# Kernel tuning notes

Hardware: AMD Instinct MI355X
Metric: run time of the kernel (lower is better)

The kernel has to match this reference:

```python
import jax, jax.numpy as jnp
import numpy as np

BS, C_IN, C_OUT, K, STYLE_DIM, BANK = 8, 64, 64, 3, 512, 4
D = H = W = 32
EPS = 1e-8
STRIDE = 1
PAD = 1


def setup_inputs() -> dict:
    key = jax.random.key(0)
    ks = jax.random.split(key, 7)
    lim_f = 1.0 / np.sqrt(STYLE_DIM)
    return {
        "x": jax.random.normal(ks[0], (BS, C_IN, D, H, W), dtype=jnp.float32),
        "w": jax.random.normal(ks[1], (BS, STYLE_DIM), dtype=jnp.float32),
        "filter_w": jax.random.uniform(ks[2], (BANK, STYLE_DIM), jnp.float32, -lim_f, lim_f),
        "filter_b": jax.random.uniform(ks[3], (BANK,), jnp.float32, -lim_f, lim_f),
        "mod_w": jax.random.uniform(ks[4], (C_IN, STYLE_DIM), jnp.float32, -lim_f, lim_f),
        "mod_b": jax.random.uniform(ks[5], (C_IN,), jnp.float32, -lim_f, lim_f),
        "bank": jax.random.normal(ks[6], (BANK, C_OUT, C_IN, K, K, K), dtype=jnp.float32),
    }


def reference(x, w, filter_w, filter_b, mod_w, mod_b, bank):
    bs, c_in, d, h, ww = x.shape
    # bank selection weights: softmax over bank axis
    fwt = jax.nn.softmax(w @ filter_w.T + filter_b, axis=-1)          # [bs, bank]
    # per-sample weights from bank (bank layout: n, out, in, k, k, k)
    weighted = jnp.einsum('bn,noijkl->boijkl', fwt, bank)             # [bs, out, in, k, k, k]
    # style modulation over input channels
    mod = (w @ mod_w.T + mod_b).reshape(bs, 1, c_in, 1, 1, 1)
    mw = weighted * mod
    # demodulation: normalize each (sample, out-channel) filter
    demod = jax.lax.rsqrt(jnp.sum(mw * mw, axis=(2, 3, 4, 5), keepdims=True) + EPS)
    mw = mw * demod
    # grouped conv with groups = bs
    mw = mw.reshape(bs * C_OUT, c_in, K, K, K)
    xr = x.reshape(1, bs * c_in, d, h, ww)
    out = jax.lax.conv_general_dilated(
        xr, mw,
        window_strides=(STRIDE,) * 3,
        padding=[(PAD, PAD)] * 3,
        dimension_numbers=('NCDHW', 'OIDHW', 'NCDHW'),
        feature_group_count=bs,
    )
    return out.reshape(bs, C_OUT, out.shape[-3], out.shape[-2], out.shape[-1])
```

## Files before the change

kernel.cpp:

```cpp
#include <hip/hip_runtime.h>
#include <math.h>

#define BS 8
#define CIN 64
#define COUT 64
#define SDIM 512
#define NBANK 4
#define DSZ 32
#define SPATIAL (DSZ*DSZ*DSZ)
#define NTAP 27
#define CH 8
#define NCH 8
#define KPAD 232
#define NKS 7
constexpr float EPS = 1e-8f;

typedef short bf16x8 __attribute__((ext_vector_type(8)));
typedef float f32x4 __attribute__((ext_vector_type(4)));

#define WA_ELEMS (BS*NCH*COUT*KPAD)

__device__ inline unsigned short bf16r(float f) {
    unsigned u = __float_as_uint(f);
    u = (u + 0x7fffu + ((u >> 16) & 1u)) >> 16;
    return (unsigned short)u;
}
__device__ inline unsigned pack2(float a, float b) {
    unsigned ua = __float_as_uint(a);
    unsigned ub = __float_as_uint(b);
    ua = (ua + 0x7fffu + ((ua >> 16) & 1u)) >> 16;
    ub = (ub + 0x7fffu + ((ub >> 16) & 1u)) & 0xffff0000u;
    return ua | ub;
}

__global__ void prep_style(const float* __restrict__ w,
                           const float* __restrict__ filter_w,
                           const float* __restrict__ filter_b,
                           const float* __restrict__ mod_w,
                           const float* __restrict__ mod_b,
                           float* __restrict__ fwt,
                           float* __restrict__ mod) {
    const int b = blockIdx.x;
    const int t = threadIdx.x;
    const float* wb = w + b * SDIM;
    __shared__ float lg[NBANK];

    if (t < NBANK) {
        float s = filter_b[t];
        const float* fr = filter_w + t * SDIM;
        for (int j = 0; j < SDIM; ++j) s += wb[j] * fr[j];
        lg[t] = s;
    }
    __syncthreads();
    if (t == 0) {
        float m = lg[0];
        for (int n = 1; n < NBANK; ++n) m = fmaxf(m, lg[n]);
        float e[NBANK];
        float s = 0.0f;
        for (int n = 0; n < NBANK; ++n) { e[n] = expf(lg[n] - m); s += e[n]; }
        for (int n = 0; n < NBANK; ++n) fwt[b * NBANK + n] = e[n] / s;
    }
    {
        float s = mod_b[t];
        const float* mr = mod_w + t * SDIM;
        for (int j = 0; j < SDIM; ++j) s += wb[j] * mr[j];
        mod[b * CIN + t] = s;
    }
}

__global__ void prep_weights(const float* __restrict__ bank,
                             const float* __restrict__ fwt,
                             const float* __restrict__ mod,
                             unsigned short* __restrict__ wA) {
    const int oc = blockIdx.x;
    const int b  = blockIdx.y;
    const int ic = threadIdx.x;

    const float f0 = fwt[b * NBANK + 0];
    const float f1 = fwt[b * NBANK + 1];
    const float f2 = fwt[b * NBANK + 2];
    const float f3 = fwt[b * NBANK + 3];
    const float m  = mod[b * CIN + ic];

    const float* b0 = bank + (size_t)((0 * COUT + oc) * CIN + ic) * NTAP;
    const float* b1 = bank + (size_t)((1 * COUT + oc) * CIN + ic) * NTAP;
    const float* b2 = bank + (size_t)((2 * COUT + oc) * CIN + ic) * NTAP;
    const float* b3 = bank + (size_t)((3 * COUT + oc) * CIN + ic) * NTAP;

    float v[NTAP];
    float ss = 0.0f;
#pragma unroll
    for (int k = 0; k < NTAP; ++k) {
        float t = f0 * b0[k] + f1 * b1[k] + f2 * b2[k] + f3 * b3[k];
        t *= m;
        v[k] = t;
        ss += t * t;
    }
#pragma unroll
    for (int off = 32; off >= 1; off >>= 1) ss += __shfl_xor(ss, off, 64);
    const float d = rsqrtf(ss + EPS);

    const int chunk = ic >> 3, icl = ic & 7;
    unsigned short* row = wA + (size_t)(((b * NCH + chunk) * COUT) + oc) * KPAD;
#pragma unroll
    for (int k = 0; k < NTAP; ++k) row[k * CH + icl] = bf16r(v[k] * d);

    unsigned short* rz = wA + (size_t)(((b * NCH + chunk) * COUT) + oc) * KPAD;
    rz[216 + icl * 2]     = 0;
    rz[216 + icl * 2 + 1] = 0;
}

__global__ __launch_bounds__(512, 2) void conv3d_mfma(
        const float* __restrict__ x,
        const unsigned short* __restrict__ wA,
        float* __restrict__ out) {
    const int bid = blockIdx.x;
    const int b = bid & 7, z = bid >> 3;
    const int t  = threadIdx.x;
    const int ln = t & 15;
    const int hi = (t >> 4) & 3;
    const int wv = t >> 6;

    __shared__ int4 smem[3468 + 1856];
    int4* xs   = smem;
    int4* Alds = smem + 3468;
    char* Xb = (char*)xs;
    const char* Ab = (const char*)Alds;

    int offBb[NKS];
#pragma unroll
    for (int ks = 0; ks < NKS; ++ks) {
        int tap = ks * 4 + hi;
        if (tap > 26) tap = 0;
        int dz = tap / 9, r = tap - dz * 9, dy = r / 3, dx = r - dy * 3;
        offBb[ks] = (dz * 1156 + dy * 34 + dx) * 16;
    }
    int baseBb[8];
#pragma unroll
    for (int st = 0; st < 8; ++st)
        baseBb[st] = ((wv * 4 + (st >> 1)) * 34 + (st & 1) * 16 + ln) * 16;
    int baseA[4];
#pragma unroll
    for (int at = 0; at < 4; ++at)
        baseA[at] = ((at * 16 + ln) * KPAD + hi * CH) * 2;

    const int4 z4 = make_int4(0, 0, 0, 0);
    for (int p = t; p < 3468; p += 512) xs[p] = z4;

    const float* xb = x + (size_t)b * CIN * SPATIAL;
    const unsigned short* wAb = wA + (size_t)b * NCH * COUT * KPAD;

    f32x4 acc[4][8];
#pragma unroll
    for (int i = 0; i < 4; ++i)
#pragma unroll
        for (int j = 0; j < 8; ++j) acc[i][j] = (f32x4){0.f, 0.f, 0.f, 0.f};

    for (int c = 0; c < NCH; ++c) {
        __syncthreads();

        {
            const int4* srcA = (const int4*)(wAb + (size_t)c * COUT * KPAD);
#pragma unroll
            for (int it = 0; it < 4; ++it) {
                int p = t + it * 512;
                if (p < 1856) Alds[p] = srcA[p];
            }
        }

#pragma unroll
        for (int rep = 0; rep < 6; ++rep) {
            int p = t + rep * 512;
            int dz = p >> 10, rem = p & 1023;
            int zz = z + dz - 1;
            int4 v = z4;
            if (zz >= 0 && zz < DSZ) {
                const float* s = xb + (size_t)c * CH * SPATIAL + (size_t)zz * 1024 + rem;
                float f0 = s[0 * SPATIAL], f1 = s[1 * SPATIAL];
                float f2 = s[2 * SPATIAL], f3 = s[3 * SPATIAL];
                float f4 = s[4 * SPATIAL], f5 = s[5 * SPATIAL];
                float f6 = s[6 * SPATIAL], f7 = s[7 * SPATIAL];
                v.x = (int)pack2(f0, f1);
                v.y = (int)pack2(f2, f3);
                v.z = (int)pack2(f4, f5);
                v.w = (int)pack2(f6, f7);
            }
            int yy = rem >> 5, xx = rem & 31;
            xs[dz * 1156 + (yy + 1) * 34 + (xx + 1)] = v;
        }
        __syncthreads();

#pragma unroll
        for (int ks = 0; ks < NKS; ++ks) {
            bf16x8 a[4];
#pragma unroll
            for (int at = 0; at < 4; ++at)
                a[at] = *(const bf16x8*)(Ab + baseA[at] + ks * 64);
            bf16x8 bf[8];
#pragma unroll
            for (int st = 0; st < 8; ++st)
                bf[st] = *(const bf16x8*)(Xb + baseBb[st] + offBb[ks]);
#pragma unroll
            for (int at = 0; at < 4; ++at)
#pragma unroll
                for (int st = 0; st < 8; ++st)
                    acc[at][st] = __builtin_amdgcn_mfma_f32_16x16x32_bf16(
                        a[at], bf[st], acc[at][st], 0, 0, 0);
        }
    }

    float* ob = out + (size_t)b * COUT * SPATIAL + (size_t)z * 1024;
#pragma unroll
    for (int at = 0; at < 4; ++at) {
        int oc = at * 16 + hi * 4;
#pragma unroll
        for (int st = 0; st < 8; ++st) {
            int sp = (wv * 4 + (st >> 1)) * 32 + (st & 1) * 16 + ln;
#pragma unroll
            for (int r = 0; r < 4; ++r)
                ob[(size_t)(oc + r) * SPATIAL + sp] = acc[at][st][r];
        }
    }
}

extern "C" void kernel_launch(void* const* d_in, const int* in_sizes, int n_in,
                              void* d_out, int out_size, void* d_ws, size_t ws_size,
                              hipStream_t stream) {
    const float* x        = (const float*)d_in[0];
    const float* w        = (const float*)d_in[1];
    const float* filter_w = (const float*)d_in[2];
    const float* filter_b = (const float*)d_in[3];
    const float* mod_w    = (const float*)d_in[4];
    const float* mod_b    = (const float*)d_in[5];
    const float* bank     = (const float*)d_in[6];
    float* out = (float*)d_out;

    unsigned short* wA = (unsigned short*)d_ws;
    float* fwt = (float*)((char*)d_ws + (size_t)WA_ELEMS * 2);
    float* mod = fwt + BS * NBANK;

    prep_style<<<BS, 64, 0, stream>>>(w, filter_w, filter_b, mod_w, mod_b, fwt, mod);
    prep_weights<<<dim3(COUT, BS), 64, 0, stream>>>(bank, fwt, mod, wA);
    conv3d_mfma<<<256, 512, 0, stream>>>(x, wA, out);
}
```

Baseline: 89.58 us.

## Pre-pack input to padded bf16 slabs and double-buffer LDS via direct global-to-LDS loads

Adds a separate kernel that converts the fp32 input into zero-padded bf16 channel-packed slabs with a 33-wide row pitch. The conv kernel then streams each channel chunk straight into double-buffered LDS using global_load_lds, so the next chunk's load overlaps the current chunk's MFMA work. The weight rows drop their padding, and the unused final tap group is zeroed in registers instead. The per-block fp32 load and conversion work disappears, at the cost of an extra pass over memory for the packed input, twice the LDS footprint, and a padded layout that is read by the matrix loads.

New measurement: 95.93 us. 1.07x slower.

```diff
diff --git a/kernel.cpp b/kernel.cpp
--- a/kernel.cpp
+++ b/kernel.cpp
@@ -11,26 +11,37 @@
 #define NTAP 27
 #define CH 8
 #define NCH 8
-#define KPAD 232
+#define KROW 216
 #define NKS 7
+#define SLABTEX (1124*33)
+#define WINTEX 3301
+#define XSTEX 3301
+#define ATEX 1728
 constexpr float EPS = 1e-8f;
 
 typedef short bf16x8 __attribute__((ext_vector_type(8)));
 typedef float f32x4 __attribute__((ext_vector_type(4)));
 
-#define WA_ELEMS (BS*NCH*COUT*KPAD)
-
-__device__ inline unsigned short bf16r(float f) {
-    unsigned u = __float_as_uint(f);
-    u = (u + 0x7fffu + ((u >> 16) & 1u)) >> 16;
-    return (unsigned short)u;
-}
-__device__ inline unsigned pack2(float a, float b) {
+#define XP_TEXELS (64*SLABTEX)
+#define WA_TEXELS (64*ATEX)
+
+__device__ __forceinline__ unsigned pack2(float a, float b) {
     unsigned ua = __float_as_uint(a);
     unsigned ub = __float_as_uint(b);
     ua = (ua + 0x7fffu + ((ua >> 16) & 1u)) >> 16;
     ub = (ub + 0x7fffu + ((ub >> 16) & 1u)) & 0xffff0000u;
     return ua | ub;
+}
+__device__ __forceinline__ unsigned short bf16r(float f) {
+    unsigned u = __float_as_uint(f);
+    u = (u + 0x7fffu + ((u >> 16) & 1u)) >> 16;
+    return (unsigned short)u;
+}
+
+__device__ __forceinline__ void gload_lds16(const int4* g, int4* l) {
+    __builtin_amdgcn_global_load_lds(
+        (const __attribute__((address_space(1))) unsigned int*)(const void*)g,
+        (__attribute__((address_space(3))) unsigned int*)(void*)l, 16, 0, 0);
 }
 
 __global__ void prep_style(const float* __restrict__ w,
@@ -101,18 +112,45 @@
     const float d = rsqrtf(ss + EPS);
 
     const int chunk = ic >> 3, icl = ic & 7;
-    unsigned short* row = wA + (size_t)(((b * NCH + chunk) * COUT) + oc) * KPAD;
+    unsigned short* row = wA + ((size_t)((b * NCH + chunk) * COUT + oc)) * KROW;
 #pragma unroll
     for (int k = 0; k < NTAP; ++k) row[k * CH + icl] = bf16r(v[k] * d);
-
-    unsigned short* rz = wA + (size_t)(((b * NCH + chunk) * COUT) + oc) * KPAD;
-    rz[216 + icl * 2]     = 0;
-    rz[216 + icl * 2 + 1] = 0;
+}
+
+__global__ __launch_bounds__(256) void xform(const float* __restrict__ x,
+                                             int4* __restrict__ xP) {
+    const int zidx = blockIdx.x;
+    const int ch   = blockIdx.y;
+    const int b    = blockIdx.z;
+    int4* slab = xP + (size_t)(b * NCH + ch) * SLABTEX;
+    const int t = threadIdx.x;
+    const int4 z4 = make_int4(0, 0, 0, 0);
+
+    if (zidx >= 32) {
+        int base = (zidx == 32) ? 0 : 1090 * 33;
+        for (int p = t; p < 34 * 33; p += 256) slab[base + p] = z4;
+        return;
+    }
+    const float* xc = x + ((size_t)b * CIN + ch * CH) * SPATIAL + zidx * 1024;
+    int4* dst = slab + (34 + 33 * zidx) * 33;
+    for (int p = t; p < 33 * 33; p += 256) {
+        const int r  = p / 33;
+        const int cx = p - r * 33;
+        int4 v = z4;
+        if (r < 32 && cx > 0) {
+            const float* s = xc + r * 32 + (cx - 1);
+            v.x = (int)pack2(s[0 * SPATIAL], s[1 * SPATIAL]);
+            v.y = (int)pack2(s[2 * SPATIAL], s[3 * SPATIAL]);
+            v.z = (int)pack2(s[4 * SPATIAL], s[5 * SPATIAL]);
+            v.w = (int)pack2(s[6 * SPATIAL], s[7 * SPATIAL]);
+        }
+        dst[p] = v;
+    }
 }
 
 __global__ __launch_bounds__(512, 2) void conv3d_mfma(
-        const float* __restrict__ x,
-        const unsigned short* __restrict__ wA,
+        const int4* __restrict__ xP,
+        const int4* __restrict__ wA,
         float* __restrict__ out) {
     const int bid = blockIdx.x;
     const int b = bid & 7, z = bid >> 3;
@@ -121,34 +159,45 @@
     const int hi = (t >> 4) & 3;
     const int wv = t >> 6;
 
-    __shared__ int4 smem[3468 + 1856];
-    int4* xs   = smem;
-    int4* Alds = smem + 3468;
-    char* Xb = (char*)xs;
-    const char* Ab = (const char*)Alds;
-
-    int offBb[NKS];
+    __shared__ int4 smem[2 * XSTEX + 2 * ATEX + 4];
+
+    int offB[NKS];
 #pragma unroll
     for (int ks = 0; ks < NKS; ++ks) {
         int tap = ks * 4 + hi;
         if (tap > 26) tap = 0;
-        int dz = tap / 9, r = tap - dz * 9, dy = r / 3, dx = r - dy * 3;
-        offBb[ks] = (dz * 1156 + dy * 34 + dx) * 16;
-    }
-    int baseBb[8];
+        const int dz = tap / 9, r = tap - dz * 9, dy = r / 3, dx = r - dy * 3;
+        offB[ks] = (dz * 1089 + dy * 33 + dx) * 16;
+    }
+    int baseB[8];
 #pragma unroll
     for (int st = 0; st < 8; ++st)
-        baseBb[st] = ((wv * 4 + (st >> 1)) * 34 + (st & 1) * 16 + ln) * 16;
-    int baseA[4];
-#pragma unroll
-    for (int at = 0; at < 4; ++at)
-        baseA[at] = ((at * 16 + ln) * KPAD + hi * CH) * 2;
-
-    const int4 z4 = make_int4(0, 0, 0, 0);
-    for (int p = t; p < 3468; p += 512) xs[p] = z4;
-
-    const float* xb = x + (size_t)b * CIN * SPATIAL;
-    const unsigned short* wAb = wA + (size_t)b * NCH * COUT * KPAD;
+        baseB[st] = ((wv * 4 + (st >> 1)) * 33 + (st & 1) * 16 + ln) * 16;
+    const int baseA = ln * 432 + hi * 16;
+
+    const size_t slab0 = (size_t)(b * NCH) * SLABTEX;
+    const int win = z * 1089;
+
+    int4 xt, at4;
+    auto stage = [&](int c, int buf) {
+        const int4* xsrc = xP + slab0 + (size_t)c * SLABTEX + win;
+        const int4* asrc = wA + (size_t)(b * NCH + c) * ATEX;
+        int4* lx = smem + buf * XSTEX;
+        int4* la = smem + 2 * XSTEX + buf * ATEX;
+        const int wb = (t & ~63);
+#pragma unroll
+        for (int i = 0; i < 6; ++i)
+            gload_lds16(xsrc + i * 512 + t, lx + i * 512 + wb);
+#pragma unroll
+        for (int i = 0; i < 3; ++i)
+            gload_lds16(asrc + i * 512 + t, la + i * 512 + wb);
+        if (t < WINTEX - 3072) xt  = xsrc[3072 + t];
+        if (t < ATEX - 1536)   at4 = asrc[1536 + t];
+    };
+    auto wtails = [&](int buf) {
+        if (t < WINTEX - 3072) smem[buf * XSTEX + 3072 + t] = xt;
+        if (t < ATEX - 1536)   smem[2 * XSTEX + buf * ATEX + 1536 + t] = at4;
+    };
 
     f32x4 acc[4][8];
 #pragma unroll
@@ -156,66 +205,50 @@
 #pragma unroll
         for (int j = 0; j < 8; ++j) acc[i][j] = (f32x4){0.f, 0.f, 0.f, 0.f};
 
+    stage(0, 0);
+    wtails(0);
+    __syncthreads();
+
+    const bf16x8 zv = {0, 0, 0, 0, 0, 0, 0, 0};
+
     for (int c = 0; c < NCH; ++c) {
-        __syncthreads();
-
-        {
-            const int4* srcA = (const int4*)(wAb + (size_t)c * COUT * KPAD);
-#pragma unroll
-            for (int it = 0; it < 4; ++it) {
-                int p = t + it * 512;
-                if (p < 1856) Alds[p] = srcA[p];
-            }
-        }
-
-#pragma unroll
-        for (int rep = 0; rep < 6; ++rep) {
-            int p = t + rep * 512;
-            int dz = p >> 10, rem = p & 1023;
-            int zz = z + dz - 1;
-            int4 v = z4;
-            if (zz >= 0 && zz < DSZ) {
-                const float* s = xb + (size_t)c * CH * SPATIAL + (size_t)zz * 1024 + rem;
-                float f0 = s[0 * SPATIAL], f1 = s[1 * SPATIAL];
-                float f2 = s[2 * SPATIAL], f3 = s[3 * SPATIAL];
-                float f4 = s[4 * SPATIAL], f5 = s[5 * SPATIAL];
-                float f6 = s[6 * SPATIAL], f7 = s[7 * SPATIAL];
-                v.x = (int)pack2(f0, f1);
-                v.y = (int)pack2(f2, f3);
-                v.z = (int)pack2(f4, f5);
-                v.w = (int)pack2(f6, f7);
-            }
-            int yy = rem >> 5, xx = rem & 31;
-            xs[dz * 1156 + (yy + 1) * 34 + (xx + 1)] = v;
-        }
-        __syncthreads();
-
+        if (c < NCH - 1) stage(c + 1, (c + 1) & 1);
+
+        const char* Xb = (const char*)(smem + (c & 1) * XSTEX);
+        const char* Ab = (const char*)(smem + 2 * XSTEX + (c & 1) * ATEX);
 #pragma unroll
         for (int ks = 0; ks < NKS; ++ks) {
             bf16x8 a[4];
 #pragma unroll
-            for (int at = 0; at < 4; ++at)
-                a[at] = *(const bf16x8*)(Ab + baseA[at] + ks * 64);
-            bf16x8 bf[8];
+            for (int at = 0; at < 4; ++at) {
+                bf16x8 av = *(const bf16x8*)(Ab + at * 6912 + baseA + ks * 64);
+                if (ks == NKS - 1) a[at] = (hi == 3) ? zv : av;
+                else               a[at] = av;
+            }
+            bf16x8 bfr[8];
 #pragma unroll
             for (int st = 0; st < 8; ++st)
-                bf[st] = *(const bf16x8*)(Xb + baseBb[st] + offBb[ks]);
+                bfr[st] = *(const bf16x8*)(Xb + baseB[st] + offB[ks]);
 #pragma unroll
             for (int at = 0; at < 4; ++at)
 #pragma unroll
                 for (int st = 0; st < 8; ++st)
                     acc[at][st] = __builtin_amdgcn_mfma_f32_16x16x32_bf16(
-                        a[at], bf[st], acc[at][st], 0, 0, 0);
+                        a[at], bfr[st], acc[at][st], 0, 0, 0);
+        }
+        if (c < NCH - 1) {
+            wtails((c + 1) & 1);
+            __syncthreads();
         }
     }
 
     float* ob = out + (size_t)b * COUT * SPATIAL + (size_t)z * 1024;
 #pragma unroll
     for (int at = 0; at < 4; ++at) {
-        int oc = at * 16 + hi * 4;
+        const int oc = at * 16 + hi * 4;
 #pragma unroll
         for (int st = 0; st < 8; ++st) {
-            int sp = (wv * 4 + (st >> 1)) * 32 + (st & 1) * 16 + ln;
+            const int sp = (wv * 4 + (st >> 1)) * 32 + (st & 1) * 16 + ln;
 #pragma unroll
             for (int r = 0; r < 4; ++r)
                 ob[(size_t)(oc + r) * SPATIAL + sp] = acc[at][st][r];
@@ -235,11 +268,14 @@
     const float* bank     = (const float*)d_in[6];
     float* out = (float*)d_out;
 
-    unsigned short* wA = (unsigned short*)d_ws;
-    float* fwt = (float*)((char*)d_ws + (size_t)WA_ELEMS * 2);
+    int4* xP = (int4*)d_ws;
+    int4* wA = xP + XP_TEXELS;
+    float* fwt = (float*)(wA + WA_TEXELS);
     float* mod = fwt + BS * NBANK;
 
     prep_style<<<BS, 64, 0, stream>>>(w, filter_w, filter_b, mod_w, mod_b, fwt, mod);
-    prep_weights<<<dim3(COUT, BS), 64, 0, stream>>>(bank, fwt, mod, wA);
-    conv3d_mfma<<<256, 512, 0, stream>>>(x, wA, out);
-}
+    prep_weights<<<dim3(COUT, BS), 64, 0, stream>>>(bank, fwt, mod,
+                                                    (unsigned short*)wA);
+    xform<<<dim3(34, NCH, BS), 256, 0, stream>>>(x, xP);
+    conv3d_mfma<<<256, 512, 0, stream>>>(xP, wA, out);
+}
```
